# Kernel optimization log

Measured on AMD Instinct MI355X. Metric: run time of the kernel, lower is better.

The kernel has to match this reference:

```python
import jax, jax.numpy as jnp
import numpy as np

EMBED = 1024
HEADS = 16
DH = EMBED // HEADS
B, S = 2, 2048


def setup_inputs() -> dict:
    key = jax.random.key(0)
    ks = jax.random.split(key, 12)
    inp = {
        "k": jax.random.normal(ks[0], (B, S, EMBED), jnp.float32),
        "q": jax.random.normal(ks[1], (B, S, EMBED), jnp.float32),
        "v": jax.random.normal(ks[2], (B, S, EMBED), jnp.float32),
        "mask": jax.random.randint(ks[3], (B, 1, S, S), 0, 2, jnp.int32),
        # per-head projections (shared across heads, as in the torch module)
        "Wk": jax.random.normal(ks[4], (DH, DH), jnp.float32) / np.sqrt(DH),
        "bk": jnp.zeros((DH,), jnp.float32),
        "Wq": jax.random.normal(ks[5], (DH, DH), jnp.float32) / np.sqrt(DH),
        "bq": jnp.zeros((DH,), jnp.float32),
        "Wv": jax.random.normal(ks[6], (DH, DH), jnp.float32) / np.sqrt(DH),
        "bv": jnp.zeros((DH,), jnp.float32),
        "Wo": jax.random.normal(ks[7], (EMBED, EMBED), jnp.float32) / np.sqrt(EMBED),
        "bo": jnp.zeros((EMBED,), jnp.float32),
    }
    return inp


def reference(k, q, v, mask, Wk, bk, Wq, bq, Wv, bv, Wo, bo):
    b, s, _ = k.shape
    sq = q.shape[1]
    # [B,S,H,dh]
    kh = k.reshape(b, s, HEADS, DH)
    qh = q.reshape(b, sq, HEADS, DH)
    vh = v.reshape(b, s, HEADS, DH)
    # per-head linear (weight shared across heads): x @ W.T + b
    kh = kh @ Wk.T + bk
    qh = qh @ Wq.T + bq
    vh = vh @ Wv.T + bv
    # scores [B,H,Sq,Sk]
    product = jnp.einsum("bqhd,bkhd->bhqk", qh, kh)
    # masked_fill BEFORE scaling, as in the original
    product = jnp.where(mask == 0, jnp.float32(-1e20), product)
    product = product / np.sqrt(DH)
    scores = jax.nn.softmax(product, axis=-1)
    ctx = jnp.einsum("bhqk,bkhd->bqhd", scores, vh).reshape(b, sq, EMBED)
    return ctx @ Wo.T + bo
```

## Files before the change

kernel.cpp:

```cpp
#include <hip/hip_runtime.h>
#include <hip/hip_bf16.h>
#include <math.h>

#define EMBED 1024
#define HEADS 16
#define DH    64
#define BATCH 2
#define SEQ   2048

typedef __attribute__((ext_vector_type(8))) short bf16x8;
typedef __attribute__((ext_vector_type(4))) short bf16x4;
typedef __attribute__((ext_vector_type(4))) float f32x4;
typedef unsigned long long u64;

static __device__ __forceinline__ unsigned short f2bf(float x) {
    unsigned u = __builtin_bit_cast(unsigned, x);
    return (unsigned short)((u + 0x7fffu + ((u >> 16) & 1u)) >> 16);
}

__global__ __launch_bounds__(256) void proj_mfma(
    const float* __restrict__ q, const float* __restrict__ k, const float* __restrict__ v,
    const float* __restrict__ Wq, const float* __restrict__ bq,
    const float* __restrict__ Wk, const float* __restrict__ bk,
    const float* __restrict__ Wv, const float* __restrict__ bv,
    unsigned short* __restrict__ qh, unsigned short* __restrict__ kh,
    unsigned short* __restrict__ vh)
{
    const int blk = blockIdx.x;
    const int which = blockIdx.y;
    const float* x; const float* W; const float* bias; unsigned short* out;
    if (which == 0)      { x = q; W = Wq; bias = bq; out = qh; }
    else if (which == 1) { x = k; W = Wk; bias = bk; out = kh; }
    else                 { x = v; W = Wv; bias = bv; out = vh; }

    __shared__ unsigned short Xs[64 * 72];
    __shared__ unsigned short Ws[64 * 72];

    const int t  = threadIdx.x;
    const int sr = t >> 2, sp = t & 3;

    {
        const float* xsrc = x + ((size_t)blk * 64 + sr) * 64 + sp * 16;
        unsigned short o[16];
#pragma unroll
        for (int u4 = 0; u4 < 4; ++u4) {
            float4 a = ((const float4*)xsrc)[u4];
            o[u4*4+0] = f2bf(a.x); o[u4*4+1] = f2bf(a.y);
            o[u4*4+2] = f2bf(a.z); o[u4*4+3] = f2bf(a.w);
        }
        *(uint4*)&Xs[sr * 72 + sp * 16]     = *(uint4*)&o[0];
        *(uint4*)&Xs[sr * 72 + sp * 16 + 8] = *(uint4*)&o[8];
        const float* wsrc = W + (size_t)sr * 64 + sp * 16;
        unsigned short wo[16];
#pragma unroll
        for (int u4 = 0; u4 < 4; ++u4) {
            float4 a = ((const float4*)wsrc)[u4];
            wo[u4*4+0] = f2bf(a.x); wo[u4*4+1] = f2bf(a.y);
            wo[u4*4+2] = f2bf(a.z); wo[u4*4+3] = f2bf(a.w);
        }
        *(uint4*)&Ws[sr * 72 + sp * 16]     = *(uint4*)&wo[0];
        *(uint4*)&Ws[sr * 72 + sp * 16 + 8] = *(uint4*)&wo[8];
    }
    __syncthreads();

    const int w    = t >> 6;
    const int lane = t & 63;
    const int l15  = lane & 15;
    const int quad = lane >> 4;

    bf16x8 af0 = *(const bf16x8*)&Xs[(w * 16 + l15) * 72 + quad * 8];
    bf16x8 af1 = *(const bf16x8*)&Xs[(w * 16 + l15) * 72 + 32 + quad * 8];

    f32x4 acc[4];
#pragma unroll
    for (int nt = 0; nt < 4; ++nt) {
        bf16x8 bf0 = *(const bf16x8*)&Ws[(nt * 16 + l15) * 72 + quad * 8];
        bf16x8 bf1 = *(const bf16x8*)&Ws[(nt * 16 + l15) * 72 + 32 + quad * 8];
        f32x4 a = {0, 0, 0, 0};
        a = __builtin_amdgcn_mfma_f32_16x16x32_bf16(af0, bf0, a, 0, 0, 0);
        a = __builtin_amdgcn_mfma_f32_16x16x32_bf16(af1, bf1, a, 0, 0, 0);
        acc[nt] = a;
    }

    const int bsidx = blk * 4 + w;
    const int b = bsidx >> 11, s = bsidx & 2047;
#pragma unroll
    for (int nt = 0; nt < 4; ++nt) {
        const int d = nt * 16 + l15;
        const float bb = bias[d];
#pragma unroll
        for (int r = 0; r < 4; ++r) {
            const int h = quad * 4 + r;
            out[(((size_t)b * HEADS + h) * SEQ + s) * DH + d] = f2bf(acc[nt][r] + bb);
        }
    }
}

__global__ __launch_bounds__(256) void vtrans_kernel(
    const unsigned short* __restrict__ vh, unsigned short* __restrict__ vt)
{
    const int st = blockIdx.x;
    const int bh = blockIdx.y;
    __shared__ unsigned short Tt[64 * 72];

    const int t = threadIdx.x;
    const int r = t >> 2, p = t & 3;

    const unsigned short* src = vh + ((size_t)bh * SEQ + st * 64 + r) * DH + p * 16;
    *(uint4*)&Tt[r * 72 + p * 16]     = *(const uint4*)src;
    *(uint4*)&Tt[r * 72 + p * 16 + 8] = *(const uint4*)(src + 8);
    __syncthreads();

    union { unsigned short u[16]; uint4 v[2]; } o;
#pragma unroll
    for (int u = 0; u < 16; ++u) o.u[u] = Tt[(p * 16 + u) * 72 + r];
    unsigned short* dst = vt + ((size_t)bh * DH + r) * SEQ + st * 64 + p * 16;
    *(uint4*)dst       = o.v[0];
    *(uint4*)(dst + 8) = o.v[1];
}

__global__ __launch_bounds__(256) void maskpack_kernel(
    const int* __restrict__ mask, u64* __restrict__ bits)
{
    const int idx = blockIdx.x * 256 + threadIdx.x;
    const int4* src = (const int4*)(mask + (size_t)idx * 64);
    u64 w = 0;
#pragma unroll
    for (int u = 0; u < 16; ++u) {
        int4 m = src[u];
        u64 nib = (m.x != 0 ? 1ull : 0) | (m.y != 0 ? 2ull : 0) |
                  (m.z != 0 ? 4ull : 0) | (m.w != 0 ? 8ull : 0);
        w |= nib << (u * 4);
    }
    bits[idx] = w;
}

__global__ __launch_bounds__(256) void wcvt_kernel(
    const float* __restrict__ Wo, unsigned short* __restrict__ Wob)
{
    const int i = (blockIdx.x * 256 + threadIdx.x) * 8;
    float4 a = ((const float4*)(Wo + i))[0];
    float4 b = ((const float4*)(Wo + i))[1];
    unsigned short o[8] = {f2bf(a.x), f2bf(a.y), f2bf(a.z), f2bf(a.w),
                           f2bf(b.x), f2bf(b.y), f2bf(b.z), f2bf(b.w)};
    *(uint4*)(Wob + i) = *(uint4*)o;
}

__global__ __launch_bounds__(256) void attn_kernel(
    const unsigned short* __restrict__ qh, const unsigned short* __restrict__ kh,
    const unsigned short* __restrict__ vt, const u64* __restrict__ mbits,
    unsigned short* __restrict__ ctx)
{
    const int q0 = blockIdx.x * 128;
    const int bh = blockIdx.y;
    const int b  = bh >> 4;

    __shared__ unsigned short Kt[64 * 72];
    __shared__ unsigned short Vt[64 * 72];

    const int t    = threadIdx.x;
    const int w    = t >> 6;
    const int lane = t & 63;
    const int l15  = lane & 15;
    const int quad = lane >> 4;
    const int sr = t >> 2, sp = t & 3;

    bf16x8 qf[2][2];
#pragma unroll
    for (int g = 0; g < 2; ++g) {
        const unsigned short* qb =
            qh + ((size_t)bh * SEQ + q0 + w * 32 + g * 16 + l15) * DH + quad * 8;
        qf[g][0] = *(const bf16x8*)qb;
        qf[g][1] = *(const bf16x8*)(qb + 32);
    }

    f32x4 O[2][4];
#pragma unroll
    for (int g = 0; g < 2; ++g)
#pragma unroll
        for (int dt = 0; dt < 4; ++dt) O[g][dt] = f32x4{0, 0, 0, 0};
    float lsum[2] = {0.f, 0.f};

    const unsigned short* kbase = kh + (size_t)bh * SEQ * DH;
    const unsigned short* vbase = vt + (size_t)bh * DH * SEQ;
    const u64* mrow0 = mbits + ((size_t)b * SEQ + q0 + w * 32 + l15) * (SEQ / 64);
    const u64* mrow1 = mrow0 + 16 * (SEQ / 64);

    for (int kt = 0; kt < SEQ / 64; ++kt) {
        __syncthreads();
        {
            const unsigned short* ks = kbase + ((size_t)(kt * 64 + sr)) * DH + sp * 16;
            *(uint4*)&Kt[sr * 72 + sp * 16]     = *(const uint4*)ks;
            *(uint4*)&Kt[sr * 72 + sp * 16 + 8] = *(const uint4*)(ks + 8);
            const unsigned short* vs = vbase + (size_t)sr * SEQ + kt * 64 + sp * 16;
            *(uint4*)&Vt[sr * 72 + sp * 16]     = *(const uint4*)vs;
            *(uint4*)&Vt[sr * 72 + sp * 16 + 8] = *(const uint4*)(vs + 8);
        }
        const u64 mb0 = mrow0[kt];
        const u64 mb1 = mrow1[kt];
        __syncthreads();

        bf16x4 p[2][4];
#pragma unroll
        for (int st = 0; st < 4; ++st) {
            bf16x8 kf0 = *(const bf16x8*)&Kt[(st * 16 + l15) * 72 + quad * 8];
            bf16x8 kf1 = *(const bf16x8*)&Kt[(st * 16 + l15) * 72 + 32 + quad * 8];
#pragma unroll
            for (int g = 0; g < 2; ++g) {
                f32x4 sa = {0, 0, 0, 0};
                sa = __builtin_amdgcn_mfma_f32_16x16x32_bf16(kf0, qf[g][0], sa, 0, 0, 0);
                sa = __builtin_amdgcn_mfma_f32_16x16x32_bf16(kf1, qf[g][1], sa, 0, 0, 0);
                const u64 mb = g ? mb1 : mb0;
                const int bp = st * 16 + quad * 4;
                float p0 = ((mb >> (bp + 0)) & 1ull) ? __expf(fminf(sa[0] * 0.125f, 60.f)) : 0.f;
                float p1 = ((mb >> (bp + 1)) & 1ull) ? __expf(fminf(sa[1] * 0.125f, 60.f)) : 0.f;
                float p2 = ((mb >> (bp + 2)) & 1ull) ? __expf(fminf(sa[2] * 0.125f, 60.f)) : 0.f;
                float p3 = ((mb >> (bp + 3)) & 1ull) ? __expf(fminf(sa[3] * 0.125f, 60.f)) : 0.f;
                lsum[g] += (p0 + p1) + (p2 + p3);
                union { __hip_bfloat162 h2[2]; bf16x4 v; } pu;
                pu.h2[0] = __float22bfloat162_rn(make_float2(p0, p1));
                pu.h2[1] = __float22bfloat162_rn(make_float2(p2, p3));
                p[g][st] = pu.v;
            }
        }

#pragma unroll
        for (int dt = 0; dt < 4; ++dt) {
#pragma unroll
            for (int st = 0; st < 4; ++st) {
                bf16x4 vb = *(const bf16x4*)&Vt[(dt * 16 + l15) * 72 + st * 16 + quad * 4];
                O[0][dt] = __builtin_amdgcn_mfma_f32_16x16x16bf16_1k(p[0][st], vb, O[0][dt], 0, 0, 0);
                O[1][dt] = __builtin_amdgcn_mfma_f32_16x16x16bf16_1k(p[1][st], vb, O[1][dt], 0, 0, 0);
            }
        }
    }

#pragma unroll
    for (int g = 0; g < 2; ++g) {
        float lr = lsum[g];
        lr += __shfl_xor(lr, 16);
        lr += __shfl_xor(lr, 32);
        const float invl = 1.0f / lr;
        float invr[4];
#pragma unroll
        for (int r = 0; r < 4; ++r) invr[r] = __shfl(invl, quad * 4 + r);
        const size_t rbase = (size_t)bh * SEQ + q0 + w * 32 + g * 16 + quad * 4;
#pragma unroll
        for (int r = 0; r < 4; ++r) {
            unsigned short* dst = ctx + (rbase + r) * DH + l15;
            dst[0]  = f2bf(O[g][0][r] * invr[r]);
            dst[16] = f2bf(O[g][1][r] * invr[r]);
            dst[32] = f2bf(O[g][2][r] * invr[r]);
            dst[48] = f2bf(O[g][3][r] * invr[r]);
        }
    }
}

__global__ __launch_bounds__(256) void outproj_mfma(
    const unsigned short* __restrict__ ctx, const unsigned short* __restrict__ Wob,
    const float* __restrict__ bo, float* __restrict__ out)
{
    const int n0 = blockIdx.x * 64;
    const int m0 = blockIdx.y * 64;
    const int b  = m0 / SEQ;
    const int s0 = m0 % SEQ;

    __shared__ unsigned short At[64 * 72];
    __shared__ unsigned short Wt[64 * 72];

    const int t    = threadIdx.x;
    const int w    = t >> 6;
    const int lane = t & 63;
    const int l15  = lane & 15;
    const int quad = lane >> 4;
    const int sr = t >> 2, sp = t & 3;

    f32x4 acc[4] = {f32x4{0,0,0,0}, f32x4{0,0,0,0}, f32x4{0,0,0,0}, f32x4{0,0,0,0}};

    for (int kt = 0; kt < HEADS; ++kt) {
        __syncthreads();
        {
            const unsigned short* as =
                ctx + (((size_t)b * HEADS + kt) * SEQ + s0 + sr) * DH + sp * 16;
            *(uint4*)&At[sr * 72 + sp * 16]     = *(const uint4*)as;
            *(uint4*)&At[sr * 72 + sp * 16 + 8] = *(const uint4*)(as + 8);
            const unsigned short* wsrc =
                Wob + (size_t)(n0 + sr) * EMBED + kt * 64 + sp * 16;
            *(uint4*)&Wt[sr * 72 + sp * 16]     = *(const uint4*)wsrc;
            *(uint4*)&Wt[sr * 72 + sp * 16 + 8] = *(const uint4*)(wsrc + 8);
        }
        __syncthreads();

        bf16x8 bf0 = *(const bf16x8*)&Wt[(w * 16 + l15) * 72 + quad * 8];
        bf16x8 bf1 = *(const bf16x8*)&Wt[(w * 16 + l15) * 72 + 32 + quad * 8];
#pragma unroll
        for (int mt = 0; mt < 4; ++mt) {
            bf16x8 af0 = *(const bf16x8*)&At[(mt * 16 + l15) * 72 + quad * 8];
            bf16x8 af1 = *(const bf16x8*)&At[(mt * 16 + l15) * 72 + 32 + quad * 8];
            acc[mt] = __builtin_amdgcn_mfma_f32_16x16x32_bf16(af0, bf0, acc[mt], 0, 0, 0);
            acc[mt] = __builtin_amdgcn_mfma_f32_16x16x32_bf16(af1, bf1, acc[mt], 0, 0, 0);
        }
    }

    const float bv = bo[n0 + w * 16 + l15];
#pragma unroll
    for (int mt = 0; mt < 4; ++mt) {
#pragma unroll
        for (int r = 0; r < 4; ++r) {
            out[(size_t)(m0 + mt * 16 + quad * 4 + r) * EMBED + n0 + w * 16 + l15] =
                acc[mt][r] + bv;
        }
    }
}

extern "C" void kernel_launch(void* const* d_in, const int* in_sizes, int n_in,
                              void* d_out, int out_size, void* d_ws, size_t ws_size,
                              hipStream_t stream) {
    const float* k    = (const float*)d_in[0];
    const float* q    = (const float*)d_in[1];
    const float* v    = (const float*)d_in[2];
    const int*   mask = (const int*)  d_in[3];
    const float* Wk   = (const float*)d_in[4];
    const float* bk   = (const float*)d_in[5];
    const float* Wq   = (const float*)d_in[6];
    const float* bq   = (const float*)d_in[7];
    const float* Wv   = (const float*)d_in[8];
    const float* bv   = (const float*)d_in[9];
    const float* Wo   = (const float*)d_in[10];
    const float* bo   = (const float*)d_in[11];
    float* out = (float*)d_out;

    const size_t TEN = (size_t)BATCH * HEADS * SEQ * DH;
    unsigned short* qh_bf = (unsigned short*)d_ws;
    unsigned short* kh_bf = qh_bf + TEN;
    unsigned short* vh_bf = kh_bf + TEN;
    unsigned short* vt_bf = vh_bf + TEN;
    unsigned short* ctxb  = vt_bf + TEN;
    unsigned short* Wob   = ctxb + TEN;
    u64*            mbits = (u64*)(Wob + EMBED * EMBED);

    proj_mfma<<<dim3(BATCH * SEQ * HEADS / 64, 3), 256, 0, stream>>>(
        q, k, v, Wq, bq, Wk, bk, Wv, bv, qh_bf, kh_bf, vh_bf);
    vtrans_kernel<<<dim3(SEQ / 64, BATCH * HEADS), 256, 0, stream>>>(vh_bf, vt_bf);
    maskpack_kernel<<<dim3((BATCH * SEQ * (SEQ / 64)) / 256), 256, 0, stream>>>(mask, mbits);
    wcvt_kernel<<<dim3(EMBED * EMBED / (256 * 8)), 256, 0, stream>>>(Wo, Wob);
    attn_kernel<<<dim3(SEQ / 128, BATCH * HEADS), 256, 0, stream>>>(
        qh_bf, kh_bf, vt_bf, mbits, ctxb);
    outproj_mfma<<<dim3(EMBED / 64, BATCH * SEQ / 64), 256, 0, stream>>>(
        ctxb, Wob, bo, out);
}
```

Before: 260.9 us.

## Split attention key range across two half-blocks with register prefetch and reduction

The attention kernel now launches 512 threads per block: each 256-thread half processes half of the key sequence for the same 128 queries, and the halves combine partial O and row sums through shared memory at the end. K/V/mask tiles for the next iteration are prefetched into registers, overlapping global loads with compute. The grid is flattened, with bh taken from the low bits so consecutive blocks hit different heads. The exp clamp is dropped and the mask nibble extraction is simplified. This adds extra waves to hide latency, at the cost of a shared-memory reduction and higher register pressure under launch_bounds(512,4).

```diff
diff --git a/kernel.cpp b/kernel.cpp
--- a/kernel.cpp
+++ b/kernel.cpp
@@ -146,24 +146,28 @@
     *(uint4*)(Wob + i) = *(uint4*)o;
 }
 
-__global__ __launch_bounds__(256) void attn_kernel(
+__global__ __launch_bounds__(512, 4) void attn_kernel(
     const unsigned short* __restrict__ qh, const unsigned short* __restrict__ kh,
     const unsigned short* __restrict__ vt, const u64* __restrict__ mbits,
     unsigned short* __restrict__ ctx)
 {
-    const int q0 = blockIdx.x * 128;
-    const int bh = blockIdx.y;
-    const int b  = bh >> 4;
-
-    __shared__ unsigned short Kt[64 * 72];
-    __shared__ unsigned short Vt[64 * 72];
+    const int bid = blockIdx.x;
+    const int bh  = bid & 31;
+    const int q0  = (bid >> 5) * 128;
+    const int b   = bh >> 4;
+
+    __shared__ uint4 smem4[2304];
+    unsigned short* KtH = ((unsigned short*)smem4) + (threadIdx.x >> 8) * 9216;
+    unsigned short* VtH = KtH + 4608;
 
     const int t    = threadIdx.x;
-    const int w    = t >> 6;
+    const int half = t >> 8;
+    const int w    = (t >> 6) & 3;
     const int lane = t & 63;
     const int l15  = lane & 15;
     const int quad = lane >> 4;
-    const int sr = t >> 2, sp = t & 3;
+    const int t2   = t & 255;
+    const int sr   = t2 >> 2, sp = t2 & 3;
 
     bf16x8 qf[2][2];
 #pragma unroll
@@ -181,41 +185,52 @@
         for (int dt = 0; dt < 4; ++dt) O[g][dt] = f32x4{0, 0, 0, 0};
     float lsum[2] = {0.f, 0.f};
 
-    const unsigned short* kbase = kh + (size_t)bh * SEQ * DH;
-    const unsigned short* vbase = vt + (size_t)bh * DH * SEQ;
-    const u64* mrow0 = mbits + ((size_t)b * SEQ + q0 + w * 32 + l15) * (SEQ / 64);
+    const unsigned short* kbase = kh + (size_t)bh * SEQ * DH + (size_t)half * 1024 * DH;
+    const unsigned short* vbase = vt + (size_t)bh * DH * SEQ + half * 1024;
+    const u64* mrow0 = mbits + ((size_t)b * SEQ + q0 + w * 32 + l15) * (SEQ / 64) + half * 16;
     const u64* mrow1 = mrow0 + 16 * (SEQ / 64);
 
-    for (int kt = 0; kt < SEQ / 64; ++kt) {
+    uint4 pk0, pk1, pv0, pv1;
+    u64 pm0, pm1;
+    {
+        const unsigned short* ks = kbase + (size_t)sr * DH + sp * 16;
+        pk0 = *(const uint4*)ks; pk1 = *(const uint4*)(ks + 8);
+        const unsigned short* vs = vbase + (size_t)sr * SEQ + sp * 16;
+        pv0 = *(const uint4*)vs; pv1 = *(const uint4*)(vs + 8);
+        pm0 = mrow0[0]; pm1 = mrow1[0];
+    }
+
+    for (int kt = 0; kt < 16; ++kt) {
         __syncthreads();
-        {
-            const unsigned short* ks = kbase + ((size_t)(kt * 64 + sr)) * DH + sp * 16;
-            *(uint4*)&Kt[sr * 72 + sp * 16]     = *(const uint4*)ks;
-            *(uint4*)&Kt[sr * 72 + sp * 16 + 8] = *(const uint4*)(ks + 8);
-            const unsigned short* vs = vbase + (size_t)sr * SEQ + kt * 64 + sp * 16;
-            *(uint4*)&Vt[sr * 72 + sp * 16]     = *(const uint4*)vs;
-            *(uint4*)&Vt[sr * 72 + sp * 16 + 8] = *(const uint4*)(vs + 8);
-        }
-        const u64 mb0 = mrow0[kt];
-        const u64 mb1 = mrow1[kt];
+        *(uint4*)&KtH[sr * 72 + sp * 16]     = pk0;
+        *(uint4*)&KtH[sr * 72 + sp * 16 + 8] = pk1;
+        *(uint4*)&VtH[sr * 72 + sp * 16]     = pv0;
+        *(uint4*)&VtH[sr * 72 + sp * 16 + 8] = pv1;
+        const u64 mb0 = pm0, mb1 = pm1;
+        if (kt < 15) {
+            const unsigned short* ks = kbase + (size_t)((kt + 1) * 64 + sr) * DH + sp * 16;
+            pk0 = *(const uint4*)ks; pk1 = *(const uint4*)(ks + 8);
+            const unsigned short* vs = vbase + (size_t)sr * SEQ + (kt + 1) * 64 + sp * 16;
+            pv0 = *(const uint4*)vs; pv1 = *(const uint4*)(vs + 8);
+            pm0 = mrow0[kt + 1]; pm1 = mrow1[kt + 1];
+        }
         __syncthreads();
 
         bf16x4 p[2][4];
 #pragma unroll
         for (int st = 0; st < 4; ++st) {
-            bf16x8 kf0 = *(const bf16x8*)&Kt[(st * 16 + l15) * 72 + quad * 8];
-            bf16x8 kf1 = *(const bf16x8*)&Kt[(st * 16 + l15) * 72 + 32 + quad * 8];
+            bf16x8 kf0 = *(const bf16x8*)&KtH[(st * 16 + l15) * 72 + quad * 8];
+            bf16x8 kf1 = *(const bf16x8*)&KtH[(st * 16 + l15) * 72 + 32 + quad * 8];
 #pragma unroll
             for (int g = 0; g < 2; ++g) {
                 f32x4 sa = {0, 0, 0, 0};
                 sa = __builtin_amdgcn_mfma_f32_16x16x32_bf16(kf0, qf[g][0], sa, 0, 0, 0);
                 sa = __builtin_amdgcn_mfma_f32_16x16x32_bf16(kf1, qf[g][1], sa, 0, 0, 0);
-                const u64 mb = g ? mb1 : mb0;
-                const int bp = st * 16 + quad * 4;
-                float p0 = ((mb >> (bp + 0)) & 1ull) ? __expf(fminf(sa[0] * 0.125f, 60.f)) : 0.f;
-                float p1 = ((mb >> (bp + 1)) & 1ull) ? __expf(fminf(sa[1] * 0.125f, 60.f)) : 0.f;
-                float p2 = ((mb >> (bp + 2)) & 1ull) ? __expf(fminf(sa[2] * 0.125f, 60.f)) : 0.f;
-                float p3 = ((mb >> (bp + 3)) & 1ull) ? __expf(fminf(sa[3] * 0.125f, 60.f)) : 0.f;
+                const unsigned nib = (unsigned)((g ? mb1 : mb0) >> (st * 16 + quad * 4)) & 0xFu;
+                float p0 = (nib & 1u) ? __expf(sa[0] * 0.125f) : 0.f;
+                float p1 = (nib & 2u) ? __expf(sa[1] * 0.125f) : 0.f;
+                float p2 = (nib & 4u) ? __expf(sa[2] * 0.125f) : 0.f;
+                float p3 = (nib & 8u) ? __expf(sa[3] * 0.125f) : 0.f;
                 lsum[g] += (p0 + p1) + (p2 + p3);
                 union { __hip_bfloat162 h2[2]; bf16x4 v; } pu;
                 pu.h2[0] = __float22bfloat162_rn(make_float2(p0, p1));
@@ -228,30 +243,57 @@
         for (int dt = 0; dt < 4; ++dt) {
 #pragma unroll
             for (int st = 0; st < 4; ++st) {
-                bf16x4 vb = *(const bf16x4*)&Vt[(dt * 16 + l15) * 72 + st * 16 + quad * 4];
+                bf16x4 vb = *(const bf16x4*)&VtH[(dt * 16 + l15) * 72 + st * 16 + quad * 4];
                 O[0][dt] = __builtin_amdgcn_mfma_f32_16x16x16bf16_1k(p[0][st], vb, O[0][dt], 0, 0, 0);
                 O[1][dt] = __builtin_amdgcn_mfma_f32_16x16x16bf16_1k(p[1][st], vb, O[1][dt], 0, 0, 0);
             }
         }
     }
 
+    float lr[2];
 #pragma unroll
     for (int g = 0; g < 2; ++g) {
-        float lr = lsum[g];
-        lr += __shfl_xor(lr, 16);
-        lr += __shfl_xor(lr, 32);
-        const float invl = 1.0f / lr;
-        float invr[4];
-#pragma unroll
-        for (int r = 0; r < 4; ++r) invr[r] = __shfl(invl, quad * 4 + r);
-        const size_t rbase = (size_t)bh * SEQ + q0 + w * 32 + g * 16 + quad * 4;
-#pragma unroll
-        for (int r = 0; r < 4; ++r) {
-            unsigned short* dst = ctx + (rbase + r) * DH + l15;
-            dst[0]  = f2bf(O[g][0][r] * invr[r]);
-            dst[16] = f2bf(O[g][1][r] * invr[r]);
-            dst[32] = f2bf(O[g][2][r] * invr[r]);
-            dst[48] = f2bf(O[g][3][r] * invr[r]);
+        lr[g] = lsum[g];
+        lr[g] += __shfl_xor(lr[g], 16);
+        lr[g] += __shfl_xor(lr[g], 32);
+    }
+
+    float* Obuf = (float*)smem4;
+    float* Ls   = ((float*)smem4) + 128 * 66;
+
+    __syncthreads();
+    if (half == 0) {
+#pragma unroll
+        for (int g = 0; g < 2; ++g)
+#pragma unroll
+            for (int dt = 0; dt < 4; ++dt)
+#pragma unroll
+                for (int r = 0; r < 4; ++r)
+                    Obuf[(w * 32 + g * 16 + quad * 4 + r) * 66 + dt * 16 + l15] = O[g][dt][r];
+        if (quad == 0) {
+            Ls[w * 32 + l15]      = lr[0];
+            Ls[w * 32 + 16 + l15] = lr[1];
+        }
+    }
+    __syncthreads();
+    if (half == 1) {
+#pragma unroll
+        for (int g = 0; g < 2; ++g) {
+            const float ltot = lr[g] + Ls[w * 32 + g * 16 + l15];
+            const float invl = 1.0f / ltot;
+            float invr[4];
+#pragma unroll
+            for (int r = 0; r < 4; ++r) invr[r] = __shfl(invl, quad * 4 + r);
+#pragma unroll
+            for (int r = 0; r < 4; ++r) {
+                const int row = w * 32 + g * 16 + quad * 4 + r;
+                unsigned short* dst = ctx + ((size_t)bh * SEQ + q0 + row) * DH + l15;
+#pragma unroll
+                for (int dt = 0; dt < 4; ++dt) {
+                    const float val = O[g][dt][r] + Obuf[row * 66 + dt * 16 + l15];
+                    dst[dt * 16] = f2bf(val * invr[r]);
+                }
+            }
         }
     }
 }
@@ -344,7 +386,7 @@
     vtrans_kernel<<<dim3(SEQ / 64, BATCH * HEADS), 256, 0, stream>>>(vh_bf, vt_bf);
     maskpack_kernel<<<dim3((BATCH * SEQ * (SEQ / 64)) / 256), 256, 0, stream>>>(mask, mbits);
     wcvt_kernel<<<dim3(EMBED * EMBED / (256 * 8)), 256, 0, stream>>>(Wo, Wob);
-    attn_kernel<<<dim3(SEQ / 128, BATCH * HEADS), 256, 0, stream>>>(
+    attn_kernel<<<dim3((SEQ / 128) * BATCH * HEADS), 512, 0, stream>>>(
         qh_bf, kh_bf, vt_bf, mbits, ctxb);
     outproj_mfma<<<dim3(EMBED / 64, BATCH * SEQ / 64), 256, 0, stream>>>(
         ctxb, Wob, bo, out);
```

Result: faster. 255.0 us (-2.3%).
